# Kernel optimization log

Hardware: AMD Instinct MI355X
Metric: run time of the kernel (lower is better)

The kernel has to match this reference:

```python
import jax, jax.numpy as jnp
import numpy as np

N_NODES = 65536
N_GRAPHS = 32
NODES_PER_GRAPH = 2048
N_EDGES = 1048576
F_IN, H1, H2, OUT = 16, 64, 64, 12


def gcn_conv(x, src, dst, W, b, num_nodes):
    """PyG GCNConv: out = D^{-1/2} (A+I) D^{-1/2} X W + b."""
    loop = jnp.arange(num_nodes, dtype=src.dtype)
    s = jnp.concatenate([src, loop])  # sources incl. self-loops
    d = jnp.concatenate([dst, loop])  # targets incl. self-loops
    deg = jax.ops.segment_sum(jnp.ones_like(d, dtype=x.dtype), d, num_segments=num_nodes)
    dinv = jnp.where(deg > 0, jax.lax.rsqrt(deg), 0.0)
    norm = dinv[s] * dinv[d]  # [E+N]
    h = x @ W  # [N, H]
    msg = h[s] * norm[:, None]  # [E+N, H] -- dominant memory traffic
    return jax.ops.segment_sum(msg, d, num_segments=num_nodes) + b


def setup_inputs() -> dict:
    key = jax.random.key(0)
    k = jax.random.split(key, 8)
    x = jax.random.normal(k[0], (N_NODES, F_IN), dtype=jnp.float32)
    edge_index = jax.random.randint(k[1], (2, N_EDGES), 0, N_NODES, dtype=jnp.int32)
    batch = jnp.repeat(jnp.arange(N_GRAPHS, dtype=jnp.int32), NODES_PER_GRAPH)
    s1 = 1.0 / np.sqrt(F_IN)
    s2 = 1.0 / np.sqrt(H1)
    s3 = 1.0 / np.sqrt(H2 * NODES_PER_GRAPH)
    W1 = jax.random.uniform(k[2], (F_IN, H1), jnp.float32, -s1, s1)
    b1 = jnp.zeros((H1,), jnp.float32)
    W2 = jax.random.uniform(k[3], (H1, H2), jnp.float32, -s2, s2)
    b2 = jnp.zeros((H2,), jnp.float32)
    Wfc = jax.random.uniform(k[4], (H2 * NODES_PER_GRAPH, OUT), jnp.float32, -s3, s3)
    bfc = jax.random.uniform(k[5], (OUT,), jnp.float32, -s3, s3)
    return {"x": x, "edge_index": edge_index, "batch": batch,
            "W1": W1, "b1": b1, "W2": W2, "b2": b2, "Wfc": Wfc, "bfc": bfc}


def reference(x, edge_index, batch, W1, b1, W2, b2, Wfc, bfc):
    src, dst = edge_index[0], edge_index[1]
    h = gcn_conv(x, src, dst, W1, b1, N_NODES)
    h = jnp.tanh(h)  # act1 (dropout rate 0 -> identity)
    h = gcn_conv(h, src, dst, W2, b2, N_NODES)
    h = jnp.tanh(h)  # act2
    # batch is sorted with exactly NODES_PER_GRAPH nodes per graph, so the
    # per-graph masked concat is a reshape: [G, P*H2]
    h_concat = h.reshape(N_GRAPHS, NODES_PER_GRAPH * H2)
    return h_concat @ Wfc + bfc
```

## Files before the change

kernel.cpp:

```cpp
#include <hip/hip_runtime.h>
#include <hip/hip_fp16.h>

#define N_NODES 65536
#define N_EDGES 1048576
#define F_IN    16
#define H       64
#define N_GRAPHS 32
#define NPG     2048
#define OUT_F   12
#define KPG     (NPG * H)
#define CAP     4864
#define NPB     16


__global__ __launch_bounds__(256) void init_kernel(int* __restrict__ gCursor,
                                                   const float* __restrict__ bfc,
                                                   float* __restrict__ out) {
    int t = threadIdx.x;
    gCursor[t] = t * CAP;
    for (int i = t; i < N_GRAPHS * OUT_F; i += 256) out[i] = bfc[i % OUT_F];
}

__global__ __launch_bounds__(256) void binA_kernel(const int* __restrict__ src,
                                                   const int* __restrict__ dst,
                                                   int* __restrict__ gCursor,
                                                   unsigned int* __restrict__ binned) {
    __shared__ int hist[256];
    __shared__ int sc[256];
    __shared__ int bnd[257];
    __shared__ int lcur[256];
    __shared__ int blkBase[256];
    __shared__ unsigned int staged[4096];
    int t = threadIdx.x;
    hist[t] = 0; lcur[t] = 0;
    __syncthreads();
    int e0 = blockIdx.x * 4096;
    unsigned int rec[16];
#pragma unroll
    for (int i = 0; i < 16; i++) {
        int e = e0 + i * 256 + t;
        unsigned int s = (unsigned int)src[e];
        unsigned int d = (unsigned int)dst[e];
        rec[i] = s | (d << 16);
        atomicAdd(&hist[d >> 8], 1);
    }
    __syncthreads();
    int cnt = hist[t];
    if (cnt) blkBase[t] = atomicAdd(&gCursor[t], cnt);
    sc[t] = cnt;
    __syncthreads();
    for (int off = 1; off < 256; off <<= 1) {
        int v = (t >= off) ? sc[t - off] : 0;
        __syncthreads();
        sc[t] += v;
        __syncthreads();
    }
    bnd[t] = sc[t] - cnt;
    if (t == 255) bnd[256] = 4096;
    __syncthreads();
#pragma unroll
    for (int i = 0; i < 16; i++) {
        int b = rec[i] >> 24;
        int p = bnd[b] + atomicAdd(&lcur[b], 1);
        staged[p] = rec[i];
    }
    __syncthreads();
    for (int i = t; i < 4096; i += 256) {
        int lo = 0;
#pragma unroll
        for (int s = 128; s > 0; s >>= 1)
            if (bnd[lo + s] <= i) lo += s;
        binned[blkBase[lo] + (i - bnd[lo])] = staged[i];
    }
}

__global__ __launch_bounds__(256) void binB_g1_kernel(const unsigned int* __restrict__ binned,
                                                      const int* __restrict__ gCursor,
                                                      const float* __restrict__ x,
                                                      int2* __restrict__ rowinfo,
                                                      unsigned short* __restrict__ nbr,
                                                      __half2* __restrict__ g1h) {
    __shared__ int hist[256];
    __shared__ int sc[256];
    __shared__ int off[256];
    __shared__ int cur[256];
    __shared__ unsigned short outS[8192];
    int b = blockIdx.x, t = threadIdx.x;
    int base = b * CAP;
    int cnt  = gCursor[b] - base;
    hist[t] = 0; cur[t] = 0;
    __syncthreads();
    for (int i = t; i < cnt; i += 256) {
        unsigned int r = binned[base + i];
        atomicAdd(&hist[(r >> 16) & 255], 1);
    }
    __syncthreads();
    int c = hist[t];
    sc[t] = c;
    __syncthreads();
    for (int o = 1; o < 256; o <<= 1) {
        int v = (t >= o) ? sc[t - o] : 0;
        __syncthreads();
        sc[t] += v;
        __syncthreads();
    }
    off[t] = sc[t] - c;
    int nd = (b << 8) + t;
    float dv = rsqrtf((float)(c + 1));
    rowinfo[nd] = make_int2(base + sc[t] - c, c);
    {
        const float4* xr = (const float4*)(x + (size_t)nd * F_IN);
        float4 x0 = xr[0], x1 = xr[1], x2 = xr[2], x3 = xr[3];
        __half2* gr = g1h + nd * 8;
        gr[0] = __floats2half2_rn(x0.x * dv, x0.y * dv);
        gr[1] = __floats2half2_rn(x0.z * dv, x0.w * dv);
        gr[2] = __floats2half2_rn(x1.x * dv, x1.y * dv);
        gr[3] = __floats2half2_rn(x1.z * dv, x1.w * dv);
        gr[4] = __floats2half2_rn(x2.x * dv, x2.y * dv);
        gr[5] = __floats2half2_rn(x2.z * dv, x2.w * dv);
        gr[6] = __floats2half2_rn(x3.x * dv, x3.y * dv);
        gr[7] = __floats2half2_rn(x3.z * dv, x3.w * dv);
    }
    __syncthreads();
    for (int i = t; i < cnt; i += 256) {
        unsigned int r = binned[base + i];
        int n = (r >> 16) & 255;
        int p = off[n] + atomicAdd(&cur[n], 1);
        outS[p] = (unsigned short)(r & 0xFFFF);
    }
    __syncthreads();
    for (int i = t; i < cnt; i += 256) nbr[base + i] = outS[i];
}

__device__ __forceinline__ void add8(float* acc, float4 q) {
    union { float4 f; __half2 h[4]; } u; u.f = q;
#pragma unroll
    for (int c = 0; c < 4; c++) {
        float2 p = __half22float2(u.h[c]);
        acc[2 * c]     += p.x;
        acc[2 * c + 1] += p.y;
    }
}
__device__ __forceinline__ void add4(float* acc, float2 q) {
    union { float2 f; __half2 h[2]; } u; u.f = q;
    float2 p0 = __half22float2(u.h[0]);
    float2 p1 = __half22float2(u.h[1]);
    acc[0] += p0.x; acc[1] += p0.y; acc[2] += p1.x; acc[3] += p1.y;
}

__global__ __launch_bounds__(256) void agg1_gemm1_kernel(const __half2* __restrict__ g1h,
                                                         const int2* __restrict__ rowinfo,
                                                         const unsigned short* __restrict__ nbr,
                                                         const float* __restrict__ W1,
                                                         const float* __restrict__ b1,
                                                         __half* __restrict__ g2h) {
    const float2* g1v = (const float2*)g1h;
    __shared__ float Ws[F_IN * H];
    __shared__ float bs[H];
    int t = threadIdx.x;
    for (int i = t; i < F_IN * H; i += 256) Ws[i] = W1[i];
    if (t < H) bs[t] = b1[t];
    __syncthreads();
    int lane = t & 63;
    int w    = t >> 6;
    int f4   = lane & 3;
    int sub  = lane >> 2;
    int v    = blockIdx.x * NPB + w;
    int2 ri  = rowinfo[v];
    int nb   = (int)nbr[ri.x + lane];
#pragma unroll 1
    for (int it = 0; it < NPB / 4; ++it) {
        int vc = v;
        int r0 = ri.x, er = ri.y;
        int nbc = nb;
        float2 sq = g1v[(vc << 2) + f4];
        if (it < NPB / 4 - 1) ri = rowinfo[vc + 4];
        float acc[4] = {0.f, 0.f, 0.f, 0.f};
        int j = 0;
        for (; j + 32 <= er; j += 32) {
            int u0 = __shfl(nbc, j + sub, 64);
            int u1 = __shfl(nbc, j + 16 + sub, 64);
            float2 q0 = g1v[(u0 << 2) + f4];
            float2 q1 = g1v[(u1 << 2) + f4];
            add4(acc, q0);
            add4(acc, q1);
        }
        for (; j < er && j < 64; j += 16) {
            int idx = j + sub;
            int u = __shfl(nbc, idx < er ? idx : 0, 64);
            float2 q = g1v[(u << 2) + f4];
            if (idx < er) add4(acc, q);
        }
        for (int base = 64; base < er; base += 64) {
            int nbx = (int)nbr[r0 + base + lane];
            for (int jj = 0; jj < 64 && base + jj < er; jj += 16) {
                int idx = jj + sub;
                int u = __shfl(nbx, (base + idx) < er ? idx : 0, 64);
                float2 q = g1v[(u << 2) + f4];
                if (base + idx < er) add4(acc, q);
            }
        }
        if (it < NPB / 4 - 1) nb = (int)nbr[ri.x + lane];
#pragma unroll
        for (int i = 0; i < 4; i++) {
            acc[i] += __shfl_xor(acc[i], 4, 64);
            acc[i] += __shfl_xor(acc[i], 8, 64);
            acc[i] += __shfl_xor(acc[i], 16, 64);
            acc[i] += __shfl_xor(acc[i], 32, 64);
        }
        add4(acc, sq);
        float dv = rsqrtf((float)(er + 1));
#pragma unroll
        for (int i = 0; i < 4; i++) acc[i] *= dv;
        float s = bs[lane];
#pragma unroll
        for (int k = 0; k < F_IN; ++k) {
            float bk = __shfl(acc[k & 3], k >> 2, 64);
            s += bk * Ws[k * H + lane];
        }
        g2h[(vc << 6) + lane] = __float2half(dv * tanhf(s));
        v += 4;
    }
}

__global__ __launch_bounds__(256) void agg2_gemm2_kernel(const __half2* __restrict__ g2h,
                                                         const int2* __restrict__ rowinfo,
                                                         const unsigned short* __restrict__ nbr,
                                                         const float* __restrict__ W2,
                                                         const float* __restrict__ b2,
                                                         float* __restrict__ h2) {
    const float4* g2v = (const float4*)g2h;
    __shared__ float Ws[H * H];
    __shared__ float bs[H];
    int t = threadIdx.x;
    for (int i = t; i < H * H; i += 256) Ws[i] = W2[i];
    if (t < H) bs[t] = b2[t];
    __syncthreads();
    int lane = t & 63;
    int w    = t >> 6;
    int f8   = lane & 7;
    int sub  = lane >> 3;
    int v    = blockIdx.x * NPB + w;
    int2 ri  = rowinfo[v];
    int nb   = (int)nbr[ri.x + lane];
#pragma unroll 1
    for (int it = 0; it < NPB / 4; ++it) {
        int vc = v;
        int r0 = ri.x, er = ri.y;
        int nbc = nb;
        float4 sq = g2v[(vc << 3) + f8];
        if (it < NPB / 4 - 1) ri = rowinfo[vc + 4];
        float acc[8] = {0.f, 0.f, 0.f, 0.f, 0.f, 0.f, 0.f, 0.f};
        int j = 0;
        for (; j + 16 <= er; j += 16) {
            int u0 = __shfl(nbc, j + sub, 64);
            int u1 = __shfl(nbc, j + 8 + sub, 64);
            float4 q0 = g2v[(u0 << 3) + f8];
            float4 q1 = g2v[(u1 << 3) + f8];
            add8(acc, q0);
            add8(acc, q1);
        }
        for (; j < er && j < 64; j += 8) {
            int idx = j + sub;
            int u = __shfl(nbc, idx < er ? idx : 0, 64);
            float4 q = g2v[(u << 3) + f8];
            if (idx < er) add8(acc, q);
        }
        for (int base = 64; base < er; base += 64) {
            int nbx = (int)nbr[r0 + base + lane];
            for (int jj = 0; jj < 64 && base + jj < er; jj += 8) {
                int idx = jj + sub;
                int u = __shfl(nbx, (base + idx) < er ? idx : 0, 64);
                float4 q = g2v[(u << 3) + f8];
                if (base + idx < er) add8(acc, q);
            }
        }
        if (it < NPB / 4 - 1) nb = (int)nbr[ri.x + lane];
#pragma unroll
        for (int i = 0; i < 8; i++) {
            acc[i] += __shfl_xor(acc[i], 8, 64);
            acc[i] += __shfl_xor(acc[i], 16, 64);
            acc[i] += __shfl_xor(acc[i], 32, 64);
        }
        add8(acc, sq);
        float dv = rsqrtf((float)(er + 1));
#pragma unroll
        for (int i = 0; i < 8; i++) acc[i] *= dv;
        float s = bs[lane];
#pragma unroll
        for (int k = 0; k < H; ++k) {
            float bk = __shfl(acc[k & 7], k >> 3, 64);
            s += bk * Ws[k * H + lane];
        }
        h2[(vc << 6) + lane] = tanhf(s);
        v += 4;
    }
}

__global__ __launch_bounds__(256) void fc_kernel(const float* __restrict__ h2,
                                                 const float* __restrict__ Wfc,
                                                 float* __restrict__ out) {
    int kc = blockIdx.x & 127;
    int gg = blockIdx.x >> 7;
    int t  = threadIdx.x;
    float acc[8][12];
#pragma unroll
    for (int g = 0; g < 8; g++)
#pragma unroll
        for (int j = 0; j < OUT_F; j++) acc[g][j] = 0.f;
    const float* hbase = h2 + (size_t)gg * 8 * KPG;
#pragma unroll
    for (int i = 0; i < 4; i++) {
        int k = (kc << 10) + (i << 8) + t;
        const float4* w4 = (const float4*)(Wfc + (size_t)k * OUT_F);
        float4 w0 = w4[0], w1 = w4[1], w2 = w4[2];
        float hv[8];
#pragma unroll
        for (int g = 0; g < 8; g++) hv[g] = hbase[(size_t)g * KPG + k];
#pragma unroll
        for (int g = 0; g < 8; g++) {
            acc[g][0] += hv[g] * w0.x;  acc[g][1] += hv[g] * w0.y;
            acc[g][2] += hv[g] * w0.z;  acc[g][3] += hv[g] * w0.w;
            acc[g][4] += hv[g] * w1.x;  acc[g][5] += hv[g] * w1.y;
            acc[g][6] += hv[g] * w1.z;  acc[g][7] += hv[g] * w1.w;
            acc[g][8] += hv[g] * w2.x;  acc[g][9] += hv[g] * w2.y;
            acc[g][10] += hv[g] * w2.z; acc[g][11] += hv[g] * w2.w;
        }
    }
#pragma unroll
    for (int g = 0; g < 8; g++)
#pragma unroll
        for (int j = 0; j < OUT_F; j++) {
            float v = acc[g][j];
            v += __shfl_xor(v, 1, 64);  v += __shfl_xor(v, 2, 64);
            v += __shfl_xor(v, 4, 64);  v += __shfl_xor(v, 8, 64);
            v += __shfl_xor(v, 16, 64); v += __shfl_xor(v, 32, 64);
            acc[g][j] = v;
        }
    __shared__ float red[4][96];
    int w = t >> 6;
    if ((t & 63) == 0) {
#pragma unroll
        for (int g = 0; g < 8; g++)
#pragma unroll
            for (int j = 0; j < OUT_F; j++) red[w][g * OUT_F + j] = acc[g][j];
    }
    __syncthreads();
    if (t < 96)
        atomicAdd(&out[gg * 96 + t], red[0][t] + red[1][t] + red[2][t] + red[3][t]);
}

extern "C" void kernel_launch(void* const* d_in, const int* in_sizes, int n_in,
                              void* d_out, int out_size, void* d_ws, size_t ws_size,
                              hipStream_t stream) {
    const float* x    = (const float*)d_in[0];
    const int*   edge = (const int*)d_in[1];
    const int*   src  = edge;
    const int*   dst  = edge + N_EDGES;
    const float* W1  = (const float*)d_in[3];
    const float* b1  = (const float*)d_in[4];
    const float* W2  = (const float*)d_in[5];
    const float* b2  = (const float*)d_in[6];
    const float* Wfc = (const float*)d_in[7];
    const float* bfc = (const float*)d_in[8];
    float* out = (float*)d_out;

    char* p = (char*)d_ws;
    auto alloc = [&](size_t n) { char* r = p; p += (n + 255) & ~(size_t)255; return r; };
    int*   gCursor    = (int*)alloc(256 * 4);
    int2*  rowinfo    = (int2*)alloc((size_t)N_NODES * 8);
    unsigned short* nbr = (unsigned short*)alloc((size_t)256 * CAP * 2 + 256);
    __half* g1h       = (__half*)alloc((size_t)N_NODES * F_IN * 2);
    __half* g2h       = (__half*)alloc((size_t)N_NODES * H * 2);
    float* h2         = (float*)alloc((size_t)N_NODES * H * 4);
    unsigned int* binned = (unsigned int*)alloc((size_t)256 * CAP * 4);

    init_kernel<<<1, 256, 0, stream>>>(gCursor, bfc, out);
    binA_kernel<<<256, 256, 0, stream>>>(src, dst, gCursor, binned);
    binB_g1_kernel<<<256, 256, 0, stream>>>(binned, gCursor, x, rowinfo, nbr,
                                            (__half2*)g1h);
    agg1_gemm1_kernel<<<N_NODES / NPB, 256, 0, stream>>>((const __half2*)g1h, rowinfo, nbr,
                                                         W1, b1, g2h);
    agg2_gemm2_kernel<<<N_NODES / NPB, 256, 0, stream>>>((const __half2*)g2h, rowinfo, nbr,
                                                         W2, b2, h2);
    fc_kernel<<<512, 256, 0, stream>>>(h2, Wfc, out);
}
```

Before: 229.6 us.

## Split GCN layer-2 aggregation and fuse GEMM2, tanh and FC into one kernel

The second aggregation kernel now only writes the normalized aggregated features. A new kernel loads 16 nodes into LDS, applies W2, bias and tanh, and immediately multiplies by the matching Wfc rows, reducing into per-graph outputs with atomics. This removes the separate FC pass and the shuffle-based GEMM inside the aggregation loop. In exchange, Wfc is re-read once per graph and there are many atomics onto a small output array.

```diff
diff --git a/kernel.cpp b/kernel.cpp
--- a/kernel.cpp
+++ b/kernel.cpp
@@ -223,19 +223,12 @@
     }
 }
 
-__global__ __launch_bounds__(256) void agg2_gemm2_kernel(const __half2* __restrict__ g2h,
-                                                         const int2* __restrict__ rowinfo,
-                                                         const unsigned short* __restrict__ nbr,
-                                                         const float* __restrict__ W2,
-                                                         const float* __restrict__ b2,
-                                                         float* __restrict__ h2) {
+__global__ __launch_bounds__(256) void agg2_kernel(const __half2* __restrict__ g2h,
+                                                   const int2* __restrict__ rowinfo,
+                                                   const unsigned short* __restrict__ nbr,
+                                                   float* __restrict__ a2) {
     const float4* g2v = (const float4*)g2h;
-    __shared__ float Ws[H * H];
-    __shared__ float bs[H];
-    int t = threadIdx.x;
-    for (int i = t; i < H * H; i += 256) Ws[i] = W2[i];
-    if (t < H) bs[t] = b2[t];
-    __syncthreads();
+    int t    = threadIdx.x;
     int lane = t & 63;
     int w    = t >> 6;
     int f8   = lane & 7;
@@ -286,68 +279,78 @@
         float dv = rsqrtf((float)(er + 1));
 #pragma unroll
         for (int i = 0; i < 8; i++) acc[i] *= dv;
+        if (sub == 0) {
+            float4* dp = (float4*)(a2 + ((size_t)vc << 6) + (f8 << 3));
+            dp[0] = make_float4(acc[0], acc[1], acc[2], acc[3]);
+            dp[1] = make_float4(acc[4], acc[5], acc[6], acc[7]);
+        }
+        v += 4;
+    }
+}
+
+__global__ __launch_bounds__(256) void gemm2_fc_kernel(const float* __restrict__ a2,
+                                                       const float* __restrict__ W2,
+                                                       const float* __restrict__ b2,
+                                                       const float* __restrict__ Wfc,
+                                                       float* __restrict__ out) {
+    __shared__ float Ws[H * H];
+    __shared__ float As[16][H];
+    __shared__ float bs[H];
+    __shared__ float red[4][OUT_F];
+    int t = threadIdx.x;
+    for (int i = t; i < H * H; i += 256) Ws[i] = W2[i];
+    if (t < H) bs[t] = b2[t];
+    {
+        const float4* ap = (const float4*)(a2 + ((size_t)blockIdx.x << 10));
+        float4 q = ap[t];
+        int node = t >> 4;
+        int k    = (t & 15) << 2;
+        As[node][k]     = q.x;
+        As[node][k + 1] = q.y;
+        As[node][k + 2] = q.z;
+        As[node][k + 3] = q.w;
+    }
+    __syncthreads();
+    int lane = t & 63, w = t >> 6;
+    int v0 = blockIdx.x * 16;
+    int g  = blockIdx.x >> 7;
+    float pa[OUT_F];
+#pragma unroll
+    for (int j = 0; j < OUT_F; j++) pa[j] = 0.f;
+#pragma unroll
+    for (int it = 0; it < 4; ++it) {
+        int nloc = (it << 2) + w;
+        int v = v0 + nloc;
+        const float* ar = As[nloc];
         float s = bs[lane];
 #pragma unroll
-        for (int k = 0; k < H; ++k) {
-            float bk = __shfl(acc[k & 7], k >> 3, 64);
-            s += bk * Ws[k * H + lane];
-        }
-        h2[(vc << 6) + lane] = tanhf(s);
-        v += 4;
-    }
-}
-
-__global__ __launch_bounds__(256) void fc_kernel(const float* __restrict__ h2,
-                                                 const float* __restrict__ Wfc,
-                                                 float* __restrict__ out) {
-    int kc = blockIdx.x & 127;
-    int gg = blockIdx.x >> 7;
-    int t  = threadIdx.x;
-    float acc[8][12];
-#pragma unroll
-    for (int g = 0; g < 8; g++)
-#pragma unroll
-        for (int j = 0; j < OUT_F; j++) acc[g][j] = 0.f;
-    const float* hbase = h2 + (size_t)gg * 8 * KPG;
-#pragma unroll
-    for (int i = 0; i < 4; i++) {
-        int k = (kc << 10) + (i << 8) + t;
-        const float4* w4 = (const float4*)(Wfc + (size_t)k * OUT_F);
-        float4 w0 = w4[0], w1 = w4[1], w2 = w4[2];
-        float hv[8];
-#pragma unroll
-        for (int g = 0; g < 8; g++) hv[g] = hbase[(size_t)g * KPG + k];
-#pragma unroll
-        for (int g = 0; g < 8; g++) {
-            acc[g][0] += hv[g] * w0.x;  acc[g][1] += hv[g] * w0.y;
-            acc[g][2] += hv[g] * w0.z;  acc[g][3] += hv[g] * w0.w;
-            acc[g][4] += hv[g] * w1.x;  acc[g][5] += hv[g] * w1.y;
-            acc[g][6] += hv[g] * w1.z;  acc[g][7] += hv[g] * w1.w;
-            acc[g][8] += hv[g] * w2.x;  acc[g][9] += hv[g] * w2.y;
-            acc[g][10] += hv[g] * w2.z; acc[g][11] += hv[g] * w2.w;
-        }
-    }
-#pragma unroll
-    for (int g = 0; g < 8; g++)
-#pragma unroll
-        for (int j = 0; j < OUT_F; j++) {
-            float v = acc[g][j];
-            v += __shfl_xor(v, 1, 64);  v += __shfl_xor(v, 2, 64);
-            v += __shfl_xor(v, 4, 64);  v += __shfl_xor(v, 8, 64);
-            v += __shfl_xor(v, 16, 64); v += __shfl_xor(v, 32, 64);
-            acc[g][j] = v;
-        }
-    __shared__ float red[4][96];
-    int w = t >> 6;
-    if ((t & 63) == 0) {
-#pragma unroll
-        for (int g = 0; g < 8; g++)
-#pragma unroll
-            for (int j = 0; j < OUT_F; j++) red[w][g * OUT_F + j] = acc[g][j];
-    }
-    __syncthreads();
-    if (t < 96)
-        atomicAdd(&out[gg * 96 + t], red[0][t] + red[1][t] + red[2][t] + red[3][t]);
+        for (int k = 0; k < H; ++k) s += ar[k] * Ws[k * H + lane];
+        float hv = tanhf(s);
+        int vl = v & (NPG - 1);
+        const float4* wr = (const float4*)(Wfc + (size_t)(vl * H + lane) * OUT_F);
+        float4 w0 = wr[0], w1 = wr[1], w2 = wr[2];
+        pa[0]  += hv * w0.x;  pa[1]  += hv * w0.y;
+        pa[2]  += hv * w0.z;  pa[3]  += hv * w0.w;
+        pa[4]  += hv * w1.x;  pa[5]  += hv * w1.y;
+        pa[6]  += hv * w1.z;  pa[7]  += hv * w1.w;
+        pa[8]  += hv * w2.x;  pa[9]  += hv * w2.y;
+        pa[10] += hv * w2.z;  pa[11] += hv * w2.w;
+    }
+#pragma unroll
+    for (int j = 0; j < OUT_F; j++) {
+        float vv = pa[j];
+        vv += __shfl_xor(vv, 1, 64);  vv += __shfl_xor(vv, 2, 64);
+        vv += __shfl_xor(vv, 4, 64);  vv += __shfl_xor(vv, 8, 64);
+        vv += __shfl_xor(vv, 16, 64); vv += __shfl_xor(vv, 32, 64);
+        pa[j] = vv;
+    }
+    if (lane == 0) {
+#pragma unroll
+        for (int j = 0; j < OUT_F; j++) red[w][j] = pa[j];
+    }
+    __syncthreads();
+    if (t < OUT_F)
+        atomicAdd(&out[g * OUT_F + t], red[0][t] + red[1][t] + red[2][t] + red[3][t]);
 }
 
 extern "C" void kernel_launch(void* const* d_in, const int* in_sizes, int n_in,
@@ -372,7 +375,7 @@
     unsigned short* nbr = (unsigned short*)alloc((size_t)256 * CAP * 2 + 256);
     __half* g1h       = (__half*)alloc((size_t)N_NODES * F_IN * 2);
     __half* g2h       = (__half*)alloc((size_t)N_NODES * H * 2);
-    float* h2         = (float*)alloc((size_t)N_NODES * H * 4);
+    float* a2         = (float*)alloc((size_t)N_NODES * H * 4);
     unsigned int* binned = (unsigned int*)alloc((size_t)256 * CAP * 4);
 
     init_kernel<<<1, 256, 0, stream>>>(gCursor, bfc, out);
@@ -381,7 +384,6 @@
                                             (__half2*)g1h);
     agg1_gemm1_kernel<<<N_NODES / NPB, 256, 0, stream>>>((const __half2*)g1h, rowinfo, nbr,
                                                          W1, b1, g2h);
-    agg2_gemm2_kernel<<<N_NODES / NPB, 256, 0, stream>>>((const __half2*)g2h, rowinfo, nbr,
-                                                         W2, b2, h2);
-    fc_kernel<<<512, 256, 0, stream>>>(h2, Wfc, out);
-}
+    agg2_kernel<<<N_NODES / NPB, 256, 0, stream>>>((const __half2*)g2h, rowinfo, nbr, a2);
+    gemm2_fc_kernel<<<N_NODES / 16, 256, 0, stream>>>(a2, W2, b2, Wfc, out);
+}
```

Result: faster. 203.1 us (-11.5%).
